# Kernel tuning notes

Measured on AMD Instinct MI355X. Metric: run time of the kernel, lower is better.

The kernel has to match this reference:

```python
import jax, jax.numpy as jnp
import numpy as np

NUM_BINS = 15
N = 33_554_432  # number of samples


def setup_inputs() -> dict:
    key = jax.random.key(0)
    k1, k2 = jax.random.split(key)
    probs = jax.random.uniform(k1, (N,), dtype=jnp.float32)
    labels = jax.random.randint(k2, (N,), 0, 2, dtype=jnp.int32)
    return {"probs": probs, "labels": labels}


def reference(probs, labels):
    # bins = linspace(0,1,NUM_BINS+1); element falls in bin b iff
    # probs > b/NUM_BINS and probs <= (b+1)/NUM_BINS  =>  b = ceil(p*NUM_BINS)-1.
    n = probs.shape[0]
    idx = jnp.clip(jnp.ceil(probs * NUM_BINS).astype(jnp.int32) - 1, 0, NUM_BINS - 1)
    # elements with probs <= 0 or > 1 fall in no bin (strict lower on bin 0)
    valid = (probs > 0.0) & (probs <= 1.0)
    w = valid.astype(probs.dtype)
    counts = jax.ops.segment_sum(w, idx, num_segments=NUM_BINS)
    sum_conf = jax.ops.segment_sum(probs * w, idx, num_segments=NUM_BINS)
    sum_acc = jax.ops.segment_sum(labels.astype(probs.dtype) * w, idx, num_segments=NUM_BINS)
    denom = jnp.maximum(counts, 1.0)  # safe divide; empty bins contribute 0
    avg_conf = sum_conf / denom
    avg_acc = sum_acc / denom
    ece = jnp.sum((counts / n) * jnp.abs(avg_acc - avg_conf))
    return ece
```

## Files before the change

### kernel.cpp

```cpp
#include <hip/hip_runtime.h>

#define NUM_BINS 15
#define NB 2048
#define NT 256
#define NCOMP 45
#define INV15 0.066666667f

typedef float vfloat4 __attribute__((ext_vector_type(4)));
typedef int   vint4   __attribute__((ext_vector_type(4)));

__device__ __forceinline__ unsigned pack_elem(float pv, int lv, int* bin_out) {
    int bin = (int)ceilf(pv * 15.0f) - 1;
    bin = (min(max(bin, -1), 15)) & 15;
    *bin_out = bin;
    float x = fmaf(pv, 4096.0f, fmaf((float)bin, -4096.0f * INV15, 0.5f));
    unsigned rq = (unsigned)x;
    return ((unsigned)lv << 24) + 0x10000u + rq;
}

__device__ __forceinline__ void process4(vfloat4 p, vint4 l, unsigned* histT) {
    int b0, b1, b2, b3;
    unsigned k0 = pack_elem(p.x, l.x, &b0);
    unsigned k1 = pack_elem(p.y, l.y, &b1);
    unsigned k2 = pack_elem(p.z, l.z, &b2);
    unsigned k3 = pack_elem(p.w, l.w, &b3);
    histT[b0 << 8] += k0;
    histT[b1 << 8] += k1;
    histT[b2 << 8] += k2;
    histT[b3 << 8] += k3;
}

__global__ __launch_bounds__(NT, 8) void ece_partial(
    const float* __restrict__ probs, const int* __restrict__ labels,
    float* __restrict__ ws, int n4)
{
    __shared__ unsigned hist[16 * NT];
    const int t = threadIdx.x;

    uint4* h4 = (uint4*)hist;
#pragma unroll
    for (int i = 0; i < 4; ++i) h4[i * NT + t] = uint4{0u, 0u, 0u, 0u};
    __syncthreads();

    const int base = blockIdx.x * 4096;
    const vfloat4* __restrict__ p4 = (const vfloat4*)probs + base;
    const vint4*   __restrict__ l4 = (const vint4*)labels + base;
    unsigned* histT = hist + t;

    if (base + 4096 <= n4) {
#pragma unroll 1
        for (int j = 0; j < 4; ++j) {
            const int o = (j << 10) + t;
            vfloat4 pv0 = __builtin_nontemporal_load(&p4[o]);
            vfloat4 pv1 = __builtin_nontemporal_load(&p4[o + 256]);
            vfloat4 pv2 = __builtin_nontemporal_load(&p4[o + 512]);
            vfloat4 pv3 = __builtin_nontemporal_load(&p4[o + 768]);
            vint4   lv0 = __builtin_nontemporal_load(&l4[o]);
            vint4   lv1 = __builtin_nontemporal_load(&l4[o + 256]);
            vint4   lv2 = __builtin_nontemporal_load(&l4[o + 512]);
            vint4   lv3 = __builtin_nontemporal_load(&l4[o + 768]);
            __builtin_amdgcn_sched_barrier(0);
            process4(pv0, lv0, histT);
            process4(pv1, lv1, histT);
            process4(pv2, lv2, histT);
            process4(pv3, lv3, histT);
        }
    } else {
        for (int j = 0; j < 4; ++j)
            for (int s = 0; s < 4; ++s) {
                const int idx = (j << 10) + (s << 8) + t;
                if (base + idx < n4)
                    process4(p4[idx], l4[idx], histT);
            }
    }
    __syncthreads();

    const int r = t >> 4, s = t & 15;
    float csum = 0.f, asum = 0.f, rsum = 0.f;
#pragma unroll
    for (int k = 0; k < 16; ++k) {
        unsigned v = hist[(r << 8) + (s << 4) + k];
        asum += (float)(v >> 24);
        csum += (float)((v >> 16) & 0xFFu);
        rsum += (float)(v & 0xFFFFu);
    }
#pragma unroll
    for (int o = 8; o; o >>= 1) {
        csum += __shfl_down(csum, o);
        asum += __shfl_down(asum, o);
        rsum += __shfl_down(rsum, o);
    }
    if (s == 0 && r < NUM_BINS) {
        float conf = fmaf(csum, (float)r * INV15, rsum * 2.44140625e-4f);
        ws[r * NB + blockIdx.x]                  = csum;
        ws[(NUM_BINS + r) * NB + blockIdx.x]     = asum;
        ws[(2 * NUM_BINS + r) * NB + blockIdx.x] = conf;
    }
}

__global__ __launch_bounds__(1024) void ece_final(
    const float* __restrict__ ws, float* __restrict__ out, float n)
{
    __shared__ float sums[NCOMP];
    const int wave = threadIdx.x >> 6;
    const int lane = threadIdx.x & 63;

    for (int c = wave; c < NCOMP; c += 16) {
        const float4* row4 = (const float4*)(ws + c * NB);
        float s = 0.f;
#pragma unroll
        for (int k = 0; k < NB / 256; ++k) {
            float4 v = row4[lane + (k << 6)];
            s += (v.x + v.y) + (v.z + v.w);
        }
#pragma unroll
        for (int o = 32; o; o >>= 1) s += __shfl_down(s, o);
        if (lane == 0) sums[c] = s;
    }
    __syncthreads();

    if (threadIdx.x == 0) {
        float ece = 0.f;
#pragma unroll
        for (int b = 0; b < NUM_BINS; ++b) {
            float cnt = sums[b];
            float acc = sums[NUM_BINS + b];
            float cf  = sums[2 * NUM_BINS + b];
            float denom = fmaxf(cnt, 1.f);
            ece += (cnt / n) * fabsf(acc / denom - cf / denom);
        }
        out[0] = ece;
    }
}

extern "C" void kernel_launch(void* const* d_in, const int* in_sizes, int n_in,
                              void* d_out, int out_size, void* d_ws, size_t ws_size,
                              hipStream_t stream)
{
    const float* probs  = (const float*)d_in[0];
    const int*   labels = (const int*)d_in[1];
    const int n = in_sizes[0];

    ece_partial<<<NB, NT, 0, stream>>>(probs, labels, (float*)d_ws, n / 4);
    ece_final<<<1, 1024, 0, stream>>>((const float*)d_ws, (float*)d_out, (float)n);
}
```

Before: 255.8 us.

## Double-buffer global loads and batch shared-memory histogram updates with conflict merging

```diff
diff --git a/kernel.cpp b/kernel.cpp
--- a/kernel.cpp
+++ b/kernel.cpp
@@ -18,19 +18,51 @@
     return ((unsigned)lv << 24) + 0x10000u + rq;
 }
 
-__device__ __forceinline__ void process4(vfloat4 p, vint4 l, unsigned* histT) {
+struct Batch { vfloat4 p0, p1, p2, p3; vint4 l0, l1, l2, l3; };
+
+__device__ __forceinline__ void load_batch(Batch& b, const vfloat4* __restrict__ p4,
+                                           const vint4* __restrict__ l4, int j, int t) {
+    const int o = (j << 10) + t;
+    b.p0 = __builtin_nontemporal_load(&p4[o]);
+    b.p1 = __builtin_nontemporal_load(&p4[o + 256]);
+    b.p2 = __builtin_nontemporal_load(&p4[o + 512]);
+    b.p3 = __builtin_nontemporal_load(&p4[o + 768]);
+    b.l0 = __builtin_nontemporal_load(&l4[o]);
+    b.l1 = __builtin_nontemporal_load(&l4[o + 256]);
+    b.l2 = __builtin_nontemporal_load(&l4[o + 512]);
+    b.l3 = __builtin_nontemporal_load(&l4[o + 768]);
+}
+
+__device__ __forceinline__ void scatter4(unsigned* histT, vfloat4 p, vint4 l) {
     int b0, b1, b2, b3;
     unsigned k0 = pack_elem(p.x, l.x, &b0);
     unsigned k1 = pack_elem(p.y, l.y, &b1);
     unsigned k2 = pack_elem(p.z, l.z, &b2);
     unsigned k3 = pack_elem(p.w, l.w, &b3);
-    histT[b0 << 8] += k0;
-    histT[b1 << 8] += k1;
-    histT[b2 << 8] += k2;
-    histT[b3 << 8] += k3;
+    unsigned c0 = histT[b0 << 8];
+    unsigned c1 = histT[b1 << 8];
+    unsigned c2 = histT[b2 << 8];
+    unsigned c3 = histT[b3 << 8];
+    const bool e10 = (b1 == b0), e20 = (b2 == b0), e21 = (b2 == b1);
+    const bool e30 = (b3 == b0), e31 = (b3 == b1), e32 = (b3 == b2);
+    unsigned m1 = k1 + (e10 ? k0 : 0u);
+    unsigned m2 = k2 + (e21 ? m1 : 0u) + ((e20 && !e10) ? k0 : 0u);
+    unsigned m3 = k3 + (e32 ? m2 : 0u) + ((e31 && !e21) ? m1 : 0u)
+                     + ((e30 && !e20 && !e10) ? k0 : 0u);
+    histT[b0 << 8] = c0 + k0;
+    histT[b1 << 8] = c1 + m1;
+    histT[b2 << 8] = c2 + m2;
+    histT[b3 << 8] = c3 + m3;
 }
 
-__global__ __launch_bounds__(NT, 8) void ece_partial(
+__device__ __forceinline__ void consume(const Batch& b, unsigned* histT) {
+    scatter4(histT, b.p0, b.l0);
+    scatter4(histT, b.p1, b.l1);
+    scatter4(histT, b.p2, b.l2);
+    scatter4(histT, b.p3, b.l3);
+}
+
+__global__ __launch_bounds__(NT, 6) void ece_partial(
     const float* __restrict__ probs, const int* __restrict__ labels,
     float* __restrict__ ws, int n4)
 {
@@ -48,30 +80,27 @@
     unsigned* histT = hist + t;
 
     if (base + 4096 <= n4) {
-#pragma unroll 1
-        for (int j = 0; j < 4; ++j) {
-            const int o = (j << 10) + t;
-            vfloat4 pv0 = __builtin_nontemporal_load(&p4[o]);
-            vfloat4 pv1 = __builtin_nontemporal_load(&p4[o + 256]);
-            vfloat4 pv2 = __builtin_nontemporal_load(&p4[o + 512]);
-            vfloat4 pv3 = __builtin_nontemporal_load(&p4[o + 768]);
-            vint4   lv0 = __builtin_nontemporal_load(&l4[o]);
-            vint4   lv1 = __builtin_nontemporal_load(&l4[o + 256]);
-            vint4   lv2 = __builtin_nontemporal_load(&l4[o + 512]);
-            vint4   lv3 = __builtin_nontemporal_load(&l4[o + 768]);
-            __builtin_amdgcn_sched_barrier(0);
-            process4(pv0, lv0, histT);
-            process4(pv1, lv1, histT);
-            process4(pv2, lv2, histT);
-            process4(pv3, lv3, histT);
+        Batch A, B;
+        load_batch(A, p4, l4, 0, t);
+        load_batch(B, p4, l4, 1, t);
+        __builtin_amdgcn_sched_barrier(0);
+        consume(A, histT);
+        load_batch(A, p4, l4, 2, t);
+        __builtin_amdgcn_sched_barrier(0);
+        consume(B, histT);
+        load_batch(B, p4, l4, 3, t);
+        __builtin_amdgcn_sched_barrier(0);
+        consume(A, histT);
+        consume(B, histT);
+    } else {
+        for (int j = 0; j < 16; ++j) {
+            const int idx = (j << 8) + t;
+            if (base + idx < n4) {
+                vfloat4 p = p4[idx];
+                vint4   l = l4[idx];
+                scatter4(histT, p, l);
+            }
         }
-    } else {
-        for (int j = 0; j < 4; ++j)
-            for (int s = 0; s < 4; ++s) {
-                const int idx = (j << 10) + (s << 8) + t;
-                if (base + idx < n4)
-                    process4(p4[idx], l4[idx], histT);
-            }
     }
     __syncthreads();
 
```

Result: no change. 254.1 us (-0.7%).
